# Kernel tuning notes

Hardware: AMD Instinct MI355X
Metric: run time of the kernel (lower is better)

Reference implementation:

```python
import jax, jax.numpy as jnp
import numpy as np

MODES = 16
WIDTH = 20


def _spectral_conv(x, w_re, w_im):
    # x: (B, C, S) real. Truncated-mode spectral conv: rfft -> keep MODES ->
    # complex channel mixing -> irfft with zero-padded spectrum (numpy irfft
    # zero-pads the input spectrum to n//2+1, matching the torch zero-init out_ft).
    S = x.shape[-1]
    x_ft = jnp.fft.rfft(x, axis=-1)                      # (B, C, S//2+1) complex
    W = w_re + 1j * w_im                                  # (Cin, Cout, MODES)
    out_modes = jnp.einsum('bim,iom->bom', x_ft[:, :, :MODES], W)
    return jnp.fft.irfft(out_modes, n=S, axis=-1)         # (B, Cout, S) real


def _fno(x, point_data,
         fc0_w, fc0_b,
         sw0_re, sw0_im, w0_w, w0_b,
         sw1_re, sw1_im, w1_w, w1_b,
         sw2_re, sw2_im, w2_w, w2_b,
         sw3_re, sw3_im, w3_w, w3_b,
         fc1_w, fc1_b, fc2_w, fc2_b):
    B, S, _ = x.shape
    grid = (point_data / jnp.max(point_data)).reshape(1, S, 1)
    grid = jnp.broadcast_to(grid, (B, S, 1))
    h = jnp.concatenate([x, grid], axis=-1)               # (B, S, 2)
    h = h @ fc0_w + fc0_b                                 # (B, S, W)
    h = jnp.transpose(h, (0, 2, 1))                       # (B, W, S)
    for (sre, sim, ww, wb) in ((sw0_re, sw0_im, w0_w, w0_b),
                               (sw1_re, sw1_im, w1_w, w1_b),
                               (sw2_re, sw2_im, w2_w, w2_b),
                               (sw3_re, sw3_im, w3_w, w3_b)):
        h1 = _spectral_conv(h, sre, sim)
        h2 = jnp.einsum('bcx,oc->box', h, ww) + wb[None, :, None]  # 1x1 conv
        h = jax.nn.gelu(h1 + h2, approximate=False)
    # last layer has no gelu in torch code? It does: only first 3 followed by gelu.
    # Correction handled below.
    return h


def _fno_full(x, point_data,
              fc0_w, fc0_b,
              sw0_re, sw0_im, w0_w, w0_b,
              sw1_re, sw1_im, w1_w, w1_b,
              sw2_re, sw2_im, w2_w, w2_b,
              sw3_re, sw3_im, w3_w, w3_b,
              fc1_w, fc1_b, fc2_w, fc2_b):
    B, S, _ = x.shape
    grid = (point_data / jnp.max(point_data)).reshape(1, S, 1)
    grid = jnp.broadcast_to(grid, (B, S, 1))
    h = jnp.concatenate([x, grid], axis=-1)               # (B, S, 2)
    h = h @ fc0_w + fc0_b                                 # (B, S, W)
    h = jnp.transpose(h, (0, 2, 1))                       # (B, W, S)
    layers = ((sw0_re, sw0_im, w0_w, w0_b),
              (sw1_re, sw1_im, w1_w, w1_b),
              (sw2_re, sw2_im, w2_w, w2_b),
              (sw3_re, sw3_im, w3_w, w3_b))
    for i, (sre, sim, ww, wb) in enumerate(layers):
        h1 = _spectral_conv(h, sre, sim)
        h2 = jnp.einsum('bcx,oc->box', h, ww) + wb[None, :, None]
        h = h1 + h2
        if i < 3:  # torch: gelu after layers 0,1,2 but NOT after layer 3
            h = jax.nn.gelu(h, approximate=False)
    h = jnp.transpose(h, (0, 2, 1))                       # (B, S, W)
    h = jax.nn.gelu(h @ fc1_w + fc1_b, approximate=False)  # (B, S, 128)
    return h @ fc2_w + fc2_b                               # (B, S, 1)


def setup_inputs() -> dict:
    key = jax.random.key(0)
    ks = jax.random.split(key, 32)
    B, S, W, M, H = 32, 65536, WIDTH, MODES, 128
    scale = 1.0 / (W * W)
    d = {
        'x': jax.random.normal(ks[0], (B, S, 1), dtype=jnp.float32),
        'point_data': jax.random.uniform(ks[1], (S,), dtype=jnp.float32),
        'fc0_w': jax.random.normal(ks[2], (2, W), dtype=jnp.float32) * 0.5,
        'fc0_b': jnp.zeros((W,), dtype=jnp.float32),
        'fc1_w': jax.random.normal(ks[3], (W, H), dtype=jnp.float32) * (1.0 / np.sqrt(W)),
        'fc1_b': jnp.zeros((H,), dtype=jnp.float32),
        'fc2_w': jax.random.normal(ks[4], (H, 1), dtype=jnp.float32) * (1.0 / np.sqrt(H)),
        'fc2_b': jnp.zeros((1,), dtype=jnp.float32),
    }
    for i in range(4):
        d[f'sw{i}_re'] = scale * jax.random.uniform(ks[5 + 4 * i], (W, W, M), dtype=jnp.float32)
        d[f'sw{i}_im'] = scale * jax.random.uniform(ks[6 + 4 * i], (W, W, M), dtype=jnp.float32)
        d[f'w{i}_w'] = jax.random.normal(ks[7 + 4 * i], (W, W), dtype=jnp.float32) * (1.0 / np.sqrt(W))
        d[f'w{i}_b'] = jnp.zeros((W,), dtype=jnp.float32)
    return d


def reference(x, point_data,
              fc0_w, fc0_b,
              sw0_re, sw0_im, w0_w, w0_b,
              sw1_re, sw1_im, w1_w, w1_b,
              sw2_re, sw2_im, w2_w, w2_b,
              sw3_re, sw3_im, w3_w, w3_b,
              fc1_w, fc1_b, fc2_w, fc2_b):
    return _fno_full(x, point_data,
                     fc0_w, fc0_b,
                     sw0_re, sw0_im, w0_w, w0_b,
                     sw1_re, sw1_im, w1_w, w1_b,
                     sw2_re, sw2_im, w2_w, w2_b,
                     sw3_re, sw3_im, w3_w, w3_b,
                     fc1_w, fc1_b, fc2_w, fc2_b)
```

## Files before the change

### kernel.cpp

```cpp
#include <hip/hip_runtime.h>
#include <math.h>

#define BB 32
#define SS 65536
#define CC 20
#define NM 16
#define HH 128
#define RP 264
#define WP 64
#define NSLOT 16

using short8  = __attribute__((ext_vector_type(8))) short;
using floatx4 = __attribute__((ext_vector_type(4))) float;

__device__ __forceinline__ unsigned short f2bf(float f) {
    union { float f; unsigned u; } v; v.f = f;
    unsigned u = v.u;
    return (unsigned short)((u + 0x7FFFu + ((u >> 16) & 1u)) >> 16);
}
__device__ __forceinline__ float bf2f(unsigned short h) {
    union { unsigned u; float f; } v; v.u = ((unsigned)h) << 16; return v.f;
}
__device__ __forceinline__ unsigned short f2bflo(float a) {
    return f2bf(a - bf2f(f2bf(a)));
}
__device__ __forceinline__ unsigned pk2(unsigned short lo, unsigned short hi) {
    return (unsigned)lo | ((unsigned)hi << 16);
}

__device__ __forceinline__ float gelu_fast(float v) {
    float u = v * v;
    float inner = v * fmaf(0.0356774081f, u, 0.7978845608f);
    float e = __builtin_amdgcn_exp2f(inner * 2.8853900818f);
    float r = __builtin_amdgcn_rcpf(e + 1.0f);
    return fmaf(-v, r, v);
}

__device__ __forceinline__ void stage_A(unsigned short* AST, int tid,
                                        const unsigned* hw,
                                        const unsigned short* chi,
                                        const unsigned short* shi) {
    uint4 q;
    int sw = tid & 7;
    unsigned* base = (unsigned*)(AST + tid * 64);
    q = (uint4){hw[0], hw[1], hw[2], hw[3]};
    *(uint4*)(base + ((0 ^ sw) << 2)) = q;
    q = (uint4){hw[4], hw[5], hw[6], hw[7]};
    *(uint4*)(base + ((1 ^ sw) << 2)) = q;
    q = (uint4){hw[8], hw[9], 0x00003F80u, 0u};
    *(uint4*)(base + ((2 ^ sw) << 2)) = q;
    q = (uint4){0u, 0u, 0u, 0u};
    *(uint4*)(base + ((3 ^ sw) << 2)) = q;
    q = (uint4){pk2(chi[0],chi[1]), pk2(chi[2],chi[3]), pk2(chi[4],chi[5]), pk2(chi[6],chi[7])};
    *(uint4*)(base + ((4 ^ sw) << 2)) = q;
    q = (uint4){pk2(chi[8],chi[9]), pk2(chi[10],chi[11]), pk2(chi[12],chi[13]), pk2(chi[14],chi[15])};
    *(uint4*)(base + ((5 ^ sw) << 2)) = q;
    q = (uint4){pk2(shi[0],shi[1]), pk2(shi[2],shi[3]), pk2(shi[4],shi[5]), pk2(shi[6],shi[7])};
    *(uint4*)(base + ((6 ^ sw) << 2)) = q;
    q = (uint4){pk2(shi[8],shi[9]), pk2(shi[10],shi[11]), pk2(shi[12],shi[13]), pk2(shi[14],shi[15])};
    *(uint4*)(base + ((7 ^ sw) << 2)) = q;
}

__global__ __launch_bounds__(256) void k_prep(const float* __restrict__ pd,
                                              const float* __restrict__ w1,
                                              float* __restrict__ invmax,
                                              float* __restrict__ cP,
                                              unsigned short* __restrict__ w1Tg) {
    int bx = blockIdx.x;
    if (bx == 0) {
        __shared__ float red[256];
        int t = threadIdx.x;
        float m = -1e30f;
        for (int i = t; i < SS; i += 256) m = fmaxf(m, pd[i]);
        red[t] = m; __syncthreads();
        for (int off = 128; off > 0; off >>= 1) {
            if (t < off) red[t] = fmaxf(red[t], red[t + off]);
            __syncthreads();
        }
        if (t == 0) invmax[0] = 1.0f / red[0];
    } else if (bx <= 1280) {
        int idx = (bx - 1) * 256 + threadIdx.x;
        float4 z = {0.f, 0.f, 0.f, 0.f};
        ((float4*)cP)[idx] = z;
    } else {
        for (int idx = threadIdx.x; idx < HH * 64; idx += 256) {
            int j = idx >> 6, k = idx & 63;
            unsigned short r = 0;
            if (k < CC) r = f2bf(w1[k * HH + j]);
            else if (k >= 32 && k < 32 + CC) r = f2bflo(w1[(k - 32) * HH + j]);
            w1Tg[idx] = r;
        }
    }
}

__device__ __forceinline__ void dft_phase(unsigned short* sh_hA, unsigned short* sh_ph,
                                          int tid, float* cPdst) {
    int wave = tid >> 6, lane = tid & 63;
    int quad = lane >> 4, frow = lane & 15;
    floatx4 acc00 = {0.f,0.f,0.f,0.f}, acc01 = {0.f,0.f,0.f,0.f};
    floatx4 acc10 = {0.f,0.f,0.f,0.f}, acc11 = {0.f,0.f,0.f,0.f};
    int kb = wave * 64 + quad * 8;
    #pragma unroll
    for (int kc = 0; kc < 2; ++kc) {
        int k = kb + kc * 32;
        short8 a0 = *(const short8*)(sh_hA + frow * RP + k);
        short8 a1 = *(const short8*)(sh_hA + (16 + frow) * RP + k);
        short8 bc = *(const short8*)(sh_ph + frow * RP + k);
        short8 bs = *(const short8*)(sh_ph + (16 + frow) * RP + k);
        acc00 = __builtin_amdgcn_mfma_f32_16x16x32_bf16(a0, bc, acc00, 0, 0, 0);
        acc01 = __builtin_amdgcn_mfma_f32_16x16x32_bf16(a0, bs, acc01, 0, 0, 0);
        acc10 = __builtin_amdgcn_mfma_f32_16x16x32_bf16(a1, bc, acc10, 0, 0, 0);
        acc11 = __builtin_amdgcn_mfma_f32_16x16x32_bf16(a1, bs, acc11, 0, 0, 0);
    }
    __syncthreads();
    float* red = (float*)sh_hA;
    #pragma unroll
    for (int r = 0; r < 4; ++r) {
        red[wave * 1024 + 0 * 256 + r * 64 + lane] = acc00[r];
        red[wave * 1024 + 1 * 256 + r * 64 + lane] = acc01[r];
        red[wave * 1024 + 2 * 256 + r * 64 + lane] = acc10[r];
        red[wave * 1024 + 3 * 256 + r * 64 + lane] = acc11[r];
    }
    __syncthreads();
    #pragma unroll
    for (int ii = 0; ii < 4; ++ii) {
        int idx = ii * 256 + tid;
        float v = red[idx] + red[1024 + idx] + red[2048 + idx] + red[3072 + idx];
        int f = idx >> 8;
        int r = (idx >> 6) & 3, ln = idx & 63;
        int o = (f >> 1) * 16 + (ln >> 4) * 4 + r;
        int m = ln & 15;
        if (o < CC) atomicAdd(cPdst + (f & 1) * 320 + o * 16 + m, v);
    }
}

__global__ __launch_bounds__(256, 4) void k_fc0_dft(const float* __restrict__ x,
        const float* __restrict__ pd, const float* __restrict__ w,
        const float* __restrict__ bias, const float* __restrict__ invmax,
        unsigned* __restrict__ h2, float* __restrict__ cP0) {
    __shared__ __align__(16) unsigned short sh_hA[32 * RP];
    __shared__ __align__(16) unsigned short sh_ph[32 * RP];
    int tid = threadIdx.x;
    {
        unsigned* z = (unsigned*)(sh_hA + CC * RP);
        for (int i = tid; i < (32 - CC) * RP / 2; i += 256) z[i] = 0;
    }
    int b = blockIdx.y;
    int s = blockIdx.x * 256 + tid;
    float xv = x[(size_t)b * SS + s];
    float g  = pd[s] * invmax[0];
    unsigned* hp2 = h2 + (size_t)b * (CC / 2) * SS + s;
    float u = (float)s * (1.0f / 32768.0f);
    float s1, c1; sincospif(u, &s1, &c1);
    float cm = 1.0f, sm = 0.0f;
    #pragma unroll
    for (int m = 0; m < NM; ++m) {
        sh_ph[m * RP + tid]        = f2bf(cm);
        sh_ph[(16 + m) * RP + tid] = f2bf(sm);
        float cn = cm * c1 - sm * s1;
        sm = sm * c1 + cm * s1;
        cm = cn;
    }
    #pragma unroll
    for (int p = 0; p < CC / 2; ++p) {
        int c0 = 2 * p, c1i = 2 * p + 1;
        float v0 = xv * w[c0]  + g * w[CC + c0]  + bias[c0];
        float v1 = xv * w[c1i] + g * w[CC + c1i] + bias[c1i];
        unsigned short a0 = f2bf(v0), a1 = f2bf(v1);
        hp2[(size_t)p * SS] = (unsigned)a0 | ((unsigned)a1 << 16);
        sh_hA[c0 * RP + tid]  = a0;
        sh_hA[c1i * RP + tid] = a1;
    }
    __syncthreads();
    dft_phase(sh_hA, sh_ph, tid, cP0 + ((size_t)(blockIdx.x & (NSLOT - 1)) * BB + b) * 640);
}

__global__ __launch_bounds__(256, 4) void k_point_dft(unsigned* __restrict__ h2,
        const unsigned short* __restrict__ Bpk,
        float* __restrict__ cPn) {
    __shared__ __align__(16) unsigned short LB[2 * 32 * RP];
    unsigned short* AST   = LB;
    unsigned short* sh_hA = LB;
    unsigned short* sh_ph = LB + 32 * RP;
    int tid = threadIdx.x;
    int b = blockIdx.y;
    int s = blockIdx.x * 256 + tid;

    float u = (float)s * (1.0f / 32768.0f);
    float s1, c1; sincospif(u, &s1, &c1);
    float cm[NM], sm[NM];
    cm[0] = 1.0f; sm[0] = 0.0f;
    #pragma unroll
    for (int m = 1; m < NM; ++m) {
        cm[m] = cm[m - 1] * c1 - sm[m - 1] * s1;
        sm[m] = sm[m - 1] * c1 + cm[m - 1] * s1;
    }
    const unsigned* hp2r = h2 + (size_t)b * (CC / 2) * SS + s;
    unsigned hw[CC / 2];
    #pragma unroll
    for (int p = 0; p < CC / 2; ++p) hw[p] = hp2r[(size_t)p * SS];
    unsigned short chi[NM], shi[NM];
    #pragma unroll
    for (int m = 0; m < NM; ++m) { chi[m] = f2bf(cm[m]); shi[m] = f2bf(sm[m]); }
    stage_A(AST, tid, hw, chi, shi);

    int wave = tid >> 6, lane = tid & 63, col = lane & 15, quad = lane >> 4;
    const unsigned short* Bp = Bpk + (size_t)b * 4096;
    short8 wh0[2], wh1[2], wl0[2], wl1[2];
    #pragma unroll
    for (int cht = 0; cht < 2; ++cht) {
        int o = cht * 16 + col;
        wh0[cht] = *(const short8*)(Bp + o * 64 + quad * 8);
        wh1[cht] = *(const short8*)(Bp + o * 64 + 32 + quad * 8);
        wl0[cht] = *(const short8*)(Bp + 2048 + o * 64 + quad * 8);
        wl1[cht] = *(const short8*)(Bp + 2048 + o * 64 + 32 + quad * 8);
    }
    unsigned* h2b = h2 + (size_t)b * (CC / 2) * SS + blockIdx.x * 256;
    unsigned pkr[2][4][2];
    #pragma unroll
    for (int st = 0; st < 4; ++st) {
        int ar = wave * 64 + st * 16 + col;
        int sw = ar & 7;
        const unsigned short* abase = AST + ar * 64;
        short8 ah0 = *(const short8*)(abase + ((quad ^ sw) << 3));
        short8 ah1 = *(const short8*)(abase + (((4 + quad) ^ sw) << 3));
        #pragma unroll
        for (int cht = 0; cht < 2; ++cht) {
            floatx4 a = {0.f, 0.f, 0.f, 0.f};
            a = __builtin_amdgcn_mfma_f32_16x16x32_bf16(wh0[cht], ah0, a, 0, 0, 0);
            a = __builtin_amdgcn_mfma_f32_16x16x32_bf16(wh1[cht], ah1, a, 0, 0, 0);
            a = __builtin_amdgcn_mfma_f32_16x16x32_bf16(wl0[cht], ah0, a, 0, 0, 0);
            a = __builtin_amdgcn_mfma_f32_16x16x32_bf16(wl1[cht], ah1, a, 0, 0, 0);
            unsigned d0 = pk2(f2bf(gelu_fast(a[0])), f2bf(gelu_fast(a[1])));
            unsigned d1 = pk2(f2bf(gelu_fast(a[2])), f2bf(gelu_fast(a[3])));
            pkr[cht][st][0] = d0;
            pkr[cht][st][1] = d1;
            int p = cht * 8 + quad * 2;
            if (p < CC / 2) {
                h2b[(size_t)p * SS + ar]       = d0;
                h2b[(size_t)(p + 1) * SS + ar] = d1;
            }
        }
    }
    __syncthreads();

    {
        unsigned* z = (unsigned*)(sh_hA + CC * RP);
        #pragma unroll
        for (int i = tid; i < (32 - CC) * RP / 2; i += 256) z[i] = 0;
    }
    #pragma unroll
    for (int m = 0; m < NM; ++m) {
        sh_ph[m * RP + tid]        = f2bf(cm[m]);
        sh_ph[(16 + m) * RP + tid] = f2bf(sm[m]);
    }
    #pragma unroll
    for (int cht = 0; cht < 2; ++cht) {
        int ob = cht * 16 + quad * 4;
        if (ob < CC) {
            #pragma unroll
            for (int st = 0; st < 4; ++st) {
                int s_loc = wave * 64 + st * 16 + col;
                #pragma unroll
                for (int rp = 0; rp < 2; ++rp) {
                    unsigned d = pkr[cht][st][rp];
                    sh_hA[(ob + 2 * rp) * RP + s_loc]     = (unsigned short)(d & 0xFFFFu);
                    sh_hA[(ob + 2 * rp + 1) * RP + s_loc] = (unsigned short)(d >> 16);
                }
            }
        }
    }
    __syncthreads();
    dft_phase(sh_hA, sh_ph, tid, cPn + ((size_t)(blockIdx.x & (NSLOT - 1)) * BB + b) * 640);
}

__global__ __launch_bounds__(320) void k_mix(const float* __restrict__ cP,
                                             const float* __restrict__ wre, const float* __restrict__ wim,
                                             const float* __restrict__ ww, const float* __restrict__ wb,
                                             float* __restrict__ cA, float* __restrict__ cB,
                                             unsigned short* __restrict__ Bpk) {
    int b = blockIdx.x, tid = threadIdx.x;
    __shared__ float PQ[640];
    const float* base = cP + (size_t)b * 640;
    int i = tid >> 4, m = tid & 15;
    float sP = 0.f, sQ = 0.f;
    #pragma unroll 4
    for (int sl = 0; sl < NSLOT; ++sl) {
        sP += base[(size_t)sl * BB * 640 + tid];
        sQ += base[(size_t)sl * BB * 640 + 320 + tid];
    }
    PQ[i * 32 + m]      = sP;
    PQ[i * 32 + 16 + m] = sQ;
    __syncthreads();
    int o = i;
    float reY = 0.f, imY = 0.f;
    #pragma unroll
    for (int c = 0; c < CC; ++c) {
        float P = PQ[c * 32 + m], Q = PQ[c * 32 + 16 + m];
        float wr = wre[(size_t)(c * CC + o) * NM + m];
        float wi = wim[(size_t)(c * CC + o) * NM + m];
        reY += P * wr + Q * wi;
        imY += P * wi - Q * wr;
    }
    const float invS = 1.0f / (float)SS;
    float a, bb;
    if (m == 0) { a = reY * invS; bb = 0.0f; }
    else        { a = 2.0f * reY * invS; bb = -2.0f * imY * invS; }
    cA[(size_t)(b * CC + o) * NM + m] = a;
    cB[(size_t)(b * CC + o) * NM + m] = bb;

    unsigned short* Bp = Bpk + (size_t)b * 4096;
    for (int idx = tid; idx < 640; idx += 320) {
        int o8 = idx >> 5, k = idx & 31;
        float v = 0.f;
        if (k < CC) v = ww[o8 * CC + k];
        else if (k == CC) v = wb[o8];
        Bp[o8 * 64 + k]        = f2bf(v);
        Bp[2048 + o8 * 64 + k] = f2bflo(v);
    }
    for (int idx = tid; idx < 768; idx += 320) {
        int o8 = 20 + (idx >> 6), k = idx & 63;
        Bp[o8 * 64 + k] = 0;
        Bp[2048 + o8 * 64 + k] = 0;
    }
    Bp[o * 64 + 32 + m]        = f2bf(a);
    Bp[o * 64 + 48 + m]        = f2bf(bb);
    Bp[2048 + o * 64 + 32 + m] = f2bflo(a);
    Bp[2048 + o * 64 + 48 + m] = f2bflo(bb);
}

__global__ __launch_bounds__(256, 4) void k_point_final(const unsigned* __restrict__ h2,
        const unsigned short* __restrict__ Bpk,
        const unsigned short* __restrict__ w1Tg, const float* __restrict__ b1,
        const float* __restrict__ w2, const float* __restrict__ b2,
        float* __restrict__ out) {
    __shared__ __align__(16) unsigned short AST[256 * 64];
    unsigned short* hT = AST;
    int tid = threadIdx.x;
    int b = blockIdx.y;
    int s = blockIdx.x * 256 + tid;

    float u = (float)s * (1.0f / 32768.0f);
    float s1, c1; sincospif(u, &s1, &c1);
    float cm[NM], sm[NM];
    cm[0] = 1.0f; sm[0] = 0.0f;
    #pragma unroll
    for (int m = 1; m < NM; ++m) {
        cm[m] = cm[m - 1] * c1 - sm[m - 1] * s1;
        sm[m] = sm[m - 1] * c1 + cm[m - 1] * s1;
    }
    const unsigned* hp2r = h2 + (size_t)b * (CC / 2) * SS + s;
    unsigned hw[CC / 2];
    #pragma unroll
    for (int p = 0; p < CC / 2; ++p) hw[p] = hp2r[(size_t)p * SS];
    unsigned short chi[NM], shi[NM];
    #pragma unroll
    for (int m = 0; m < NM; ++m) { chi[m] = f2bf(cm[m]); shi[m] = f2bf(sm[m]); }
    stage_A(AST, tid, hw, chi, shi);

    int wave = tid >> 6, lane = tid & 63, col = lane & 15, quad = lane >> 4;
    const unsigned short* Bp = Bpk + (size_t)b * 4096;
    short8 wh0[2], wh1[2], wl0[2], wl1[2];
    #pragma unroll
    for (int cht = 0; cht < 2; ++cht) {
        int o = cht * 16 + col;
        wh0[cht] = *(const short8*)(Bp + o * 64 + quad * 8);
        wh1[cht] = *(const short8*)(Bp + o * 64 + 32 + quad * 8);
        wl0[cht] = *(const short8*)(Bp + 2048 + o * 64 + quad * 8);
        wl1[cht] = *(const short8*)(Bp + 2048 + o * 64 + 32 + quad * 8);
    }
    float res[2][4][4];
    #pragma unroll
    for (int st = 0; st < 4; ++st) {
        int ar = wave * 64 + st * 16 + col;
        int sw = ar & 7;
        const unsigned short* abase = AST + ar * 64;
        short8 ah0 = *(const short8*)(abase + ((quad ^ sw) << 3));
        short8 ah1 = *(const short8*)(abase + (((4 + quad) ^ sw) << 3));
        #pragma unroll
        for (int cht = 0; cht < 2; ++cht) {
            floatx4 a = {0.f, 0.f, 0.f, 0.f};
            a = __builtin_amdgcn_mfma_f32_16x16x32_bf16(wh0[cht], ah0, a, 0, 0, 0);
            a = __builtin_amdgcn_mfma_f32_16x16x32_bf16(wh1[cht], ah1, a, 0, 0, 0);
            a = __builtin_amdgcn_mfma_f32_16x16x32_bf16(wl0[cht], ah0, a, 0, 0, 0);
            a = __builtin_amdgcn_mfma_f32_16x16x32_bf16(wl1[cht], ah1, a, 0, 0, 0);
            #pragma unroll
            for (int r = 0; r < 4; ++r) res[cht][st][r] = a[r];
        }
    }

    #pragma unroll
    for (int cht = 0; cht < 2; ++cht) {
        #pragma unroll
        for (int st = 0; st < 4; ++st) {
            int row = wave * 64 + st * 16 + col;
            int sw = row & 7;
            unsigned* rb = (unsigned*)(hT + row * WP);
            #pragma unroll
            for (int rp = 0; rp < 2; ++rp) {
                int dwi = cht * 8 + quad * 2 + rp;
                if (dwi < CC / 2) {
                    float f0 = res[cht][st][2 * rp], f1 = res[cht][st][2 * rp + 1];
                    unsigned short h0 = f2bf(f0), h1 = f2bf(f1);
                    unsigned short l0 = f2bf(f0 - bf2f(h0)), l1 = f2bf(f1 - bf2f(h1));
                    int chunk = dwi >> 2, pos = dwi & 3;
                    rb[((chunk ^ sw) << 2) + pos]       = pk2(h0, h1);
                    rb[(((chunk + 4) ^ sw) << 2) + pos] = pk2(l0, l1);
                }
            }
        }
    }

    short8 bhi[8], blo[8];
    #pragma unroll
    for (int nt = 0; nt < 8; ++nt) {
        bhi[nt] = *(const short8*)(w1Tg + (size_t)(nt * 16 + col) * 64 + quad * 8);
        blo[nt] = *(const short8*)(w1Tg + (size_t)(nt * 16 + col) * 64 + 32 + quad * 8);
    }
    float lb1r[8], w2r[8];
    #pragma unroll
    for (int nt = 0; nt < 8; ++nt) { lb1r[nt] = b1[nt * 16 + col]; w2r[nt] = w2[nt * 16 + col]; }
    float b2v = b2[0];
    #pragma unroll
    for (int mt = 0; mt < 4; ++mt) {
        int srow = wave * 64 + mt * 16 + col;
        int sw = srow & 7;
        short8 ahi = *(const short8*)(hT + srow * WP + ((quad ^ sw) << 3));
        short8 alo = *(const short8*)(hT + srow * WP + (((quad ^ sw) ^ 4) << 3));
        float part[4] = {0.f, 0.f, 0.f, 0.f};
        #pragma unroll
        for (int nt = 0; nt < 8; ++nt) {
            floatx4 a = {0.f, 0.f, 0.f, 0.f};
            a = __builtin_amdgcn_mfma_f32_16x16x32_bf16(ahi, bhi[nt], a, 0, 0, 0);
            a = __builtin_amdgcn_mfma_f32_16x16x32_bf16(ahi, blo[nt], a, 0, 0, 0);
            a = __builtin_amdgcn_mfma_f32_16x16x32_bf16(alo, bhi[nt], a, 0, 0, 0);
            #pragma unroll
            for (int r = 0; r < 4; ++r) {
                float t = gelu_fast(a[r] + lb1r[nt]);
                part[r] += t * w2r[nt];
            }
        }
        #pragma unroll
        for (int r = 0; r < 4; ++r) {
            float p = part[r];
            p += __shfl_xor(p, 1, 64);
            p += __shfl_xor(p, 2, 64);
            p += __shfl_xor(p, 4, 64);
            p += __shfl_xor(p, 8, 64);
            if (col == 0) {
                int row = wave * 64 + mt * 16 + quad * 4 + r;
                *(float*)(&hT[row * WP + ((row & 7) << 3)]) = p + b2v;
            }
        }
    }
    __syncthreads();
    out[(size_t)b * SS + blockIdx.x * 256 + tid] = *(const float*)(&hT[tid * WP + ((tid & 7) << 3)]);
}

extern "C" void kernel_launch(void* const* d_in, const int* in_sizes, int n_in,
                              void* d_out, int out_size, void* d_ws, size_t ws_size,
                              hipStream_t stream) {
    (void)in_sizes; (void)n_in; (void)out_size; (void)ws_size;
    const float* x    = (const float*)d_in[0];
    const float* pd   = (const float*)d_in[1];
    const float* fc0w = (const float*)d_in[2];
    const float* fc0b = (const float*)d_in[3];
    const float* fc1w = (const float*)d_in[4];
    const float* fc1b = (const float*)d_in[5];
    const float* fc2w = (const float*)d_in[6];
    const float* fc2b = (const float*)d_in[7];

    char* ws = (char*)d_ws;
    unsigned* h2 = (unsigned*)ws;
    size_t off = (size_t)BB * (CC / 2) * SS * 4;
    float* cP = (float*)(ws + off); off += (size_t)4 * NSLOT * BB * 640 * 4;
    float* cA = (float*)(ws + off); off += (size_t)BB * CC * NM * 4;
    float* cB = (float*)(ws + off); off += (size_t)BB * CC * NM * 4;
    float* invmax = (float*)(ws + off); off += 256;
    unsigned short* w1Tg = (unsigned short*)(ws + off); off += (size_t)HH * 64 * 2;
    unsigned short* Bpk  = (unsigned short*)(ws + off); off += (size_t)BB * 4096 * 2;
    const size_t CPL = (size_t)NSLOT * BB * 640;

    dim3 gBS(SS / 256, BB);

    k_prep<<<1282, 256, 0, stream>>>(pd, fc1w, invmax, cP, w1Tg);
    k_fc0_dft<<<gBS, 256, 0, stream>>>(x, pd, fc0w, fc0b, invmax, h2, cP);

    for (int l = 0; l < 3; ++l) {
        const float* wre = (const float*)d_in[8 + 4 * l];
        const float* wim = (const float*)d_in[9 + 4 * l];
        const float* ww  = (const float*)d_in[10 + 4 * l];
        const float* wb  = (const float*)d_in[11 + 4 * l];
        k_mix<<<BB, 320, 0, stream>>>(cP + (size_t)l * CPL, wre, wim, ww, wb, cA, cB, Bpk);
        k_point_dft<<<gBS, 256, 0, stream>>>(h2, Bpk, cP + (size_t)(l + 1) * CPL);
    }
    {
        const float* wre = (const float*)d_in[20];
        const float* wim = (const float*)d_in[21];
        const float* ww  = (const float*)d_in[22];
        const float* wb  = (const float*)d_in[23];
        k_mix<<<BB, 320, 0, stream>>>(cP + (size_t)3 * CPL, wre, wim, ww, wb, cA, cB, Bpk);
        k_point_final<<<gBS, 256, 0, stream>>>(h2, Bpk,
                                               w1Tg, fc1b, fc2w, fc2b, (float*)d_out);
    }
}
```

Baseline: 548.8 us.

## Precompute bf16 twiddle table once and fold fc1 bias into MFMA

A new set of k_prep blocks computes the per-position bf16 cos/sin values for the 16 modes once and stores them in a workspace table. The fc0, point-DFT and final kernels now load 64 bytes per position from that table instead of running sincospi and a 16-step recurrence plus conversions. In the final kernel the fc1 bias is folded into the MFMA by appending a constant-1 channel to the activations and the bias as an extra weight row, and the 16-lane reduction uses DPP row shifts in place of xor shuffles. The trade is about 4 MB of extra table reads for each of the five point kernels in exchange for less ALU work.

```diff
diff --git a/kernel.cpp b/kernel.cpp
--- a/kernel.cpp
+++ b/kernel.cpp
@@ -36,36 +36,38 @@
     return fmaf(-v, r, v);
 }
 
+__device__ __forceinline__ float row16_sum(float p) {
+    union { float f; int i; } v, w;
+    v.f = p;
+    w.i = __builtin_amdgcn_update_dpp(0, v.i, 0x121, 0xF, 0xF, true); v.f += w.f;
+    w.i = __builtin_amdgcn_update_dpp(0, v.i, 0x122, 0xF, 0xF, true); v.f += w.f;
+    w.i = __builtin_amdgcn_update_dpp(0, v.i, 0x124, 0xF, 0xF, true); v.f += w.f;
+    w.i = __builtin_amdgcn_update_dpp(0, v.i, 0x128, 0xF, 0xF, true); v.f += w.f;
+    return v.f;
+}
+
 __device__ __forceinline__ void stage_A(unsigned short* AST, int tid,
                                         const unsigned* hw,
-                                        const unsigned short* chi,
-                                        const unsigned short* shi) {
-    uint4 q;
+                                        uint4 tc0, uint4 tc1, uint4 ts0, uint4 ts1) {
     int sw = tid & 7;
     unsigned* base = (unsigned*)(AST + tid * 64);
-    q = (uint4){hw[0], hw[1], hw[2], hw[3]};
-    *(uint4*)(base + ((0 ^ sw) << 2)) = q;
-    q = (uint4){hw[4], hw[5], hw[6], hw[7]};
-    *(uint4*)(base + ((1 ^ sw) << 2)) = q;
-    q = (uint4){hw[8], hw[9], 0x00003F80u, 0u};
-    *(uint4*)(base + ((2 ^ sw) << 2)) = q;
-    q = (uint4){0u, 0u, 0u, 0u};
-    *(uint4*)(base + ((3 ^ sw) << 2)) = q;
-    q = (uint4){pk2(chi[0],chi[1]), pk2(chi[2],chi[3]), pk2(chi[4],chi[5]), pk2(chi[6],chi[7])};
-    *(uint4*)(base + ((4 ^ sw) << 2)) = q;
-    q = (uint4){pk2(chi[8],chi[9]), pk2(chi[10],chi[11]), pk2(chi[12],chi[13]), pk2(chi[14],chi[15])};
-    *(uint4*)(base + ((5 ^ sw) << 2)) = q;
-    q = (uint4){pk2(shi[0],shi[1]), pk2(shi[2],shi[3]), pk2(shi[4],shi[5]), pk2(shi[6],shi[7])};
-    *(uint4*)(base + ((6 ^ sw) << 2)) = q;
-    q = (uint4){pk2(shi[8],shi[9]), pk2(shi[10],shi[11]), pk2(shi[12],shi[13]), pk2(shi[14],shi[15])};
-    *(uint4*)(base + ((7 ^ sw) << 2)) = q;
+    *(uint4*)(base + ((0 ^ sw) << 2)) = (uint4){hw[0], hw[1], hw[2], hw[3]};
+    *(uint4*)(base + ((1 ^ sw) << 2)) = (uint4){hw[4], hw[5], hw[6], hw[7]};
+    *(uint4*)(base + ((2 ^ sw) << 2)) = (uint4){hw[8], hw[9], 0x00003F80u, 0u};
+    *(uint4*)(base + ((3 ^ sw) << 2)) = (uint4){0u, 0u, 0u, 0u};
+    *(uint4*)(base + ((4 ^ sw) << 2)) = tc0;
+    *(uint4*)(base + ((5 ^ sw) << 2)) = tc1;
+    *(uint4*)(base + ((6 ^ sw) << 2)) = ts0;
+    *(uint4*)(base + ((7 ^ sw) << 2)) = ts1;
 }
 
 __global__ __launch_bounds__(256) void k_prep(const float* __restrict__ pd,
                                               const float* __restrict__ w1,
+                                              const float* __restrict__ b1f,
                                               float* __restrict__ invmax,
                                               float* __restrict__ cP,
-                                              unsigned short* __restrict__ w1Tg) {
+                                              unsigned short* __restrict__ w1Tg,
+                                              unsigned* __restrict__ trigT) {
     int bx = blockIdx.x;
     if (bx == 0) {
         __shared__ float red[256];
@@ -82,14 +84,34 @@
         int idx = (bx - 1) * 256 + threadIdx.x;
         float4 z = {0.f, 0.f, 0.f, 0.f};
         ((float4*)cP)[idx] = z;
-    } else {
+    } else if (bx == 1281) {
         for (int idx = threadIdx.x; idx < HH * 64; idx += 256) {
             int j = idx >> 6, k = idx & 63;
             unsigned short r = 0;
             if (k < CC) r = f2bf(w1[k * HH + j]);
+            else if (k == CC) r = f2bf(b1f[j]);
             else if (k >= 32 && k < 32 + CC) r = f2bflo(w1[(k - 32) * HH + j]);
+            else if (k == 32 + CC) r = f2bflo(b1f[j]);
             w1Tg[idx] = r;
         }
+    } else {
+        int s = (bx - 1282) * 256 + threadIdx.x;
+        float u = (float)s * (1.0f / 32768.0f);
+        float s1, c1; sincospif(u, &s1, &c1);
+        float cm = 1.0f, sm = 0.0f;
+        unsigned short ch[NM], sh[NM];
+        #pragma unroll
+        for (int m = 0; m < NM; ++m) {
+            ch[m] = f2bf(cm); sh[m] = f2bf(sm);
+            float cn = cm * c1 - sm * s1;
+            sm = sm * c1 + cm * s1;
+            cm = cn;
+        }
+        uint4* row = (uint4*)(trigT + (size_t)s * 16);
+        row[0] = (uint4){pk2(ch[0],ch[1]), pk2(ch[2],ch[3]), pk2(ch[4],ch[5]), pk2(ch[6],ch[7])};
+        row[1] = (uint4){pk2(ch[8],ch[9]), pk2(ch[10],ch[11]), pk2(ch[12],ch[13]), pk2(ch[14],ch[15])};
+        row[2] = (uint4){pk2(sh[0],sh[1]), pk2(sh[2],sh[3]), pk2(sh[4],sh[5]), pk2(sh[6],sh[7])};
+        row[3] = (uint4){pk2(sh[8],sh[9]), pk2(sh[10],sh[11]), pk2(sh[12],sh[13]), pk2(sh[14],sh[15])};
     }
 }
 
@@ -137,6 +159,7 @@
 __global__ __launch_bounds__(256, 4) void k_fc0_dft(const float* __restrict__ x,
         const float* __restrict__ pd, const float* __restrict__ w,
         const float* __restrict__ bias, const float* __restrict__ invmax,
+        const unsigned* __restrict__ trigT,
         unsigned* __restrict__ h2, float* __restrict__ cP0) {
     __shared__ __align__(16) unsigned short sh_hA[32 * RP];
     __shared__ __align__(16) unsigned short sh_ph[32 * RP];
@@ -150,16 +173,15 @@
     float xv = x[(size_t)b * SS + s];
     float g  = pd[s] * invmax[0];
     unsigned* hp2 = h2 + (size_t)b * (CC / 2) * SS + s;
-    float u = (float)s * (1.0f / 32768.0f);
-    float s1, c1; sincospif(u, &s1, &c1);
-    float cm = 1.0f, sm = 0.0f;
+    const uint4* trow = (const uint4*)(trigT + (size_t)s * 16);
+    uint4 tc0 = trow[0], tc1 = trow[1], ts0 = trow[2], ts1 = trow[3];
+    unsigned c8[8] = {tc0.x, tc0.y, tc0.z, tc0.w, tc1.x, tc1.y, tc1.z, tc1.w};
+    unsigned s8[8] = {ts0.x, ts0.y, ts0.z, ts0.w, ts1.x, ts1.y, ts1.z, ts1.w};
     #pragma unroll
     for (int m = 0; m < NM; ++m) {
-        sh_ph[m * RP + tid]        = f2bf(cm);
-        sh_ph[(16 + m) * RP + tid] = f2bf(sm);
-        float cn = cm * c1 - sm * s1;
-        sm = sm * c1 + cm * s1;
-        cm = cn;
+        unsigned cd = c8[m >> 1], sd = s8[m >> 1];
+        sh_ph[m * RP + tid]        = (unsigned short)((m & 1) ? (cd >> 16) : (cd & 0xFFFFu));
+        sh_ph[(16 + m) * RP + tid] = (unsigned short)((m & 1) ? (sd >> 16) : (sd & 0xFFFFu));
     }
     #pragma unroll
     for (int p = 0; p < CC / 2; ++p) {
@@ -177,6 +199,7 @@
 
 __global__ __launch_bounds__(256, 4) void k_point_dft(unsigned* __restrict__ h2,
         const unsigned short* __restrict__ Bpk,
+        const unsigned* __restrict__ trigT,
         float* __restrict__ cPn) {
     __shared__ __align__(16) unsigned short LB[2 * 32 * RP];
     unsigned short* AST   = LB;
@@ -186,23 +209,13 @@
     int b = blockIdx.y;
     int s = blockIdx.x * 256 + tid;
 
-    float u = (float)s * (1.0f / 32768.0f);
-    float s1, c1; sincospif(u, &s1, &c1);
-    float cm[NM], sm[NM];
-    cm[0] = 1.0f; sm[0] = 0.0f;
-    #pragma unroll
-    for (int m = 1; m < NM; ++m) {
-        cm[m] = cm[m - 1] * c1 - sm[m - 1] * s1;
-        sm[m] = sm[m - 1] * c1 + cm[m - 1] * s1;
-    }
+    const uint4* trow = (const uint4*)(trigT + (size_t)s * 16);
+    uint4 tc0 = trow[0], tc1 = trow[1], ts0 = trow[2], ts1 = trow[3];
     const unsigned* hp2r = h2 + (size_t)b * (CC / 2) * SS + s;
     unsigned hw[CC / 2];
     #pragma unroll
     for (int p = 0; p < CC / 2; ++p) hw[p] = hp2r[(size_t)p * SS];
-    unsigned short chi[NM], shi[NM];
-    #pragma unroll
-    for (int m = 0; m < NM; ++m) { chi[m] = f2bf(cm[m]); shi[m] = f2bf(sm[m]); }
-    stage_A(AST, tid, hw, chi, shi);
+    stage_A(AST, tid, hw, tc0, tc1, ts0, ts1);
 
     int wave = tid >> 6, lane = tid & 63, col = lane & 15, quad = lane >> 4;
     const unsigned short* Bp = Bpk + (size_t)b * 4096;
@@ -249,10 +262,15 @@
         #pragma unroll
         for (int i = tid; i < (32 - CC) * RP / 2; i += 256) z[i] = 0;
     }
-    #pragma unroll
-    for (int m = 0; m < NM; ++m) {
-        sh_ph[m * RP + tid]        = f2bf(cm[m]);
-        sh_ph[(16 + m) * RP + tid] = f2bf(sm[m]);
+    {
+        unsigned c8[8] = {tc0.x, tc0.y, tc0.z, tc0.w, tc1.x, tc1.y, tc1.z, tc1.w};
+        unsigned s8[8] = {ts0.x, ts0.y, ts0.z, ts0.w, ts1.x, ts1.y, ts1.z, ts1.w};
+        #pragma unroll
+        for (int m = 0; m < NM; ++m) {
+            unsigned cd = c8[m >> 1], sd = s8[m >> 1];
+            sh_ph[m * RP + tid]        = (unsigned short)((m & 1) ? (cd >> 16) : (cd & 0xFFFFu));
+            sh_ph[(16 + m) * RP + tid] = (unsigned short)((m & 1) ? (sd >> 16) : (sd & 0xFFFFu));
+        }
     }
     #pragma unroll
     for (int cht = 0; cht < 2; ++cht) {
@@ -331,8 +349,9 @@
 
 __global__ __launch_bounds__(256, 4) void k_point_final(const unsigned* __restrict__ h2,
         const unsigned short* __restrict__ Bpk,
-        const unsigned short* __restrict__ w1Tg, const float* __restrict__ b1,
+        const unsigned short* __restrict__ w1Tg,
         const float* __restrict__ w2, const float* __restrict__ b2,
+        const unsigned* __restrict__ trigT,
         float* __restrict__ out) {
     __shared__ __align__(16) unsigned short AST[256 * 64];
     unsigned short* hT = AST;
@@ -340,23 +359,13 @@
     int b = blockIdx.y;
     int s = blockIdx.x * 256 + tid;
 
-    float u = (float)s * (1.0f / 32768.0f);
-    float s1, c1; sincospif(u, &s1, &c1);
-    float cm[NM], sm[NM];
-    cm[0] = 1.0f; sm[0] = 0.0f;
-    #pragma unroll
-    for (int m = 1; m < NM; ++m) {
-        cm[m] = cm[m - 1] * c1 - sm[m - 1] * s1;
-        sm[m] = sm[m - 1] * c1 + cm[m - 1] * s1;
-    }
+    const uint4* trow = (const uint4*)(trigT + (size_t)s * 16);
+    uint4 tc0 = trow[0], tc1 = trow[1], ts0 = trow[2], ts1 = trow[3];
     const unsigned* hp2r = h2 + (size_t)b * (CC / 2) * SS + s;
     unsigned hw[CC / 2];
     #pragma unroll
     for (int p = 0; p < CC / 2; ++p) hw[p] = hp2r[(size_t)p * SS];
-    unsigned short chi[NM], shi[NM];
-    #pragma unroll
-    for (int m = 0; m < NM; ++m) { chi[m] = f2bf(cm[m]); shi[m] = f2bf(sm[m]); }
-    stage_A(AST, tid, hw, chi, shi);
+    stage_A(AST, tid, hw, tc0, tc1, ts0, ts1);
 
     int wave = tid >> 6, lane = tid & 63, col = lane & 15, quad = lane >> 4;
     const unsigned short* Bp = Bpk + (size_t)b * 4096;
@@ -399,8 +408,10 @@
             #pragma unroll
             for (int rp = 0; rp < 2; ++rp) {
                 int dwi = cht * 8 + quad * 2 + rp;
-                if (dwi < CC / 2) {
-                    float f0 = res[cht][st][2 * rp], f1 = res[cht][st][2 * rp + 1];
+                if (dwi <= CC / 2) {
+                    float f0, f1;
+                    if (dwi == CC / 2) { f0 = 1.0f; f1 = 0.0f; }
+                    else { f0 = res[cht][st][2 * rp]; f1 = res[cht][st][2 * rp + 1]; }
                     unsigned short h0 = f2bf(f0), h1 = f2bf(f1);
                     unsigned short l0 = f2bf(f0 - bf2f(h0)), l1 = f2bf(f1 - bf2f(h1));
                     int chunk = dwi >> 2, pos = dwi & 3;
@@ -417,9 +428,9 @@
         bhi[nt] = *(const short8*)(w1Tg + (size_t)(nt * 16 + col) * 64 + quad * 8);
         blo[nt] = *(const short8*)(w1Tg + (size_t)(nt * 16 + col) * 64 + 32 + quad * 8);
     }
-    float lb1r[8], w2r[8];
-    #pragma unroll
-    for (int nt = 0; nt < 8; ++nt) { lb1r[nt] = b1[nt * 16 + col]; w2r[nt] = w2[nt * 16 + col]; }
+    float w2r[8];
+    #pragma unroll
+    for (int nt = 0; nt < 8; ++nt) w2r[nt] = w2[nt * 16 + col];
     float b2v = b2[0];
     #pragma unroll
     for (int mt = 0; mt < 4; ++mt) {
@@ -436,17 +447,13 @@
             a = __builtin_amdgcn_mfma_f32_16x16x32_bf16(alo, bhi[nt], a, 0, 0, 0);
             #pragma unroll
             for (int r = 0; r < 4; ++r) {
-                float t = gelu_fast(a[r] + lb1r[nt]);
+                float t = gelu_fast(a[r]);
                 part[r] += t * w2r[nt];
             }
         }
         #pragma unroll
         for (int r = 0; r < 4; ++r) {
-            float p = part[r];
-            p += __shfl_xor(p, 1, 64);
-            p += __shfl_xor(p, 2, 64);
-            p += __shfl_xor(p, 4, 64);
-            p += __shfl_xor(p, 8, 64);
+            float p = row16_sum(part[r]);
             if (col == 0) {
                 int row = wave * 64 + mt * 16 + quad * 4 + r;
                 *(float*)(&hT[row * WP + ((row & 7) << 3)]) = p + b2v;
@@ -479,12 +486,13 @@
     float* invmax = (float*)(ws + off); off += 256;
     unsigned short* w1Tg = (unsigned short*)(ws + off); off += (size_t)HH * 64 * 2;
     unsigned short* Bpk  = (unsigned short*)(ws + off); off += (size_t)BB * 4096 * 2;
+    unsigned* trigT = (unsigned*)(ws + off); off += (size_t)SS * 16 * 4;
     const size_t CPL = (size_t)NSLOT * BB * 640;
 
     dim3 gBS(SS / 256, BB);
 
-    k_prep<<<1282, 256, 0, stream>>>(pd, fc1w, invmax, cP, w1Tg);
-    k_fc0_dft<<<gBS, 256, 0, stream>>>(x, pd, fc0w, fc0b, invmax, h2, cP);
+    k_prep<<<1538, 256, 0, stream>>>(pd, fc1w, fc1b, invmax, cP, w1Tg, trigT);
+    k_fc0_dft<<<gBS, 256, 0, stream>>>(x, pd, fc0w, fc0b, invmax, trigT, h2, cP);
 
     for (int l = 0; l < 3; ++l) {
         const float* wre = (const float*)d_in[8 + 4 * l];
@@ -492,7 +500,7 @@
         const float* ww  = (const float*)d_in[10 + 4 * l];
         const float* wb  = (const float*)d_in[11 + 4 * l];
         k_mix<<<BB, 320, 0, stream>>>(cP + (size_t)l * CPL, wre, wim, ww, wb, cA, cB, Bpk);
-        k_point_dft<<<gBS, 256, 0, stream>>>(h2, Bpk, cP + (size_t)(l + 1) * CPL);
+        k_point_dft<<<gBS, 256, 0, stream>>>(h2, Bpk, trigT, cP + (size_t)(l + 1) * CPL);
     }
     {
         const float* wre = (const float*)d_in[20];
@@ -500,7 +508,6 @@
         const float* ww  = (const float*)d_in[22];
         const float* wb  = (const float*)d_in[23];
         k_mix<<<BB, 320, 0, stream>>>(cP + (size_t)3 * CPL, wre, wim, ww, wb, cA, cB, Bpk);
-        k_point_final<<<gBS, 256, 0, stream>>>(h2, Bpk,
-                                               w1Tg, fc1b, fc2w, fc2b, (float*)d_out);
-    }
-}
+        k_point_final<<<gBS, 256, 0, stream>>>(h2, Bpk, w1Tg, fc2w, fc2b, trigT, (float*)d_out);
+    }
+}
```

Result: faster. 531.8 us (-3.1%).
